# Kernel tuning notes

Measured on AMD Instinct MI355X. Metric: run time of the kernel, lower is better.

Reference implementation:

```python
import jax, jax.numpy as jnp
import numpy as np

MARGIN = 1.0
EPS = 1e-12


def setup_inputs() -> dict:
    key = jax.random.key(0)
    k1, k2, k3 = jax.random.split(key, 3)
    B, C, D = 16384, 500, 512
    features = jax.random.normal(k1, (B, D), dtype=jnp.float32)
    prototypes = jax.random.normal(k2, (C, D), dtype=jnp.float32)
    labels = jax.random.randint(k3, (B,), 0, C, dtype=jnp.int64)
    return {"features": features, "prototypes": prototypes, "labels": labels}


def reference(features, prototypes, labels):
    # Pairwise L2 distances [B, C] via the expanded form (no [B,C,D] intermediate)
    f2 = jnp.sum(features * features, axis=-1, keepdims=True)   # [B, 1]
    p2 = jnp.sum(prototypes * prototypes, axis=-1)               # [C]
    sq = f2 + p2 - 2.0 * (features @ prototypes.T)               # [B, C]
    dists = jnp.sqrt(jnp.maximum(sq, EPS))                       # [B, C]

    B, C = dists.shape
    d_pos = jnp.take_along_axis(dists, labels[:, None], axis=1)[:, 0]  # [B]
    pos_mask = jax.nn.one_hot(labels, C, dtype=bool)             # [B, C]
    d_neg_min = jnp.min(jnp.where(pos_mask, jnp.inf, dists), axis=-1)  # [B]

    loss = jnp.mean(jax.nn.relu(d_pos - d_neg_min + MARGIN))
    return loss
```

## Files before the change

### kernel.cpp

```cpp
#include <hip/hip_runtime.h>
#include <stdint.h>
#include <stddef.h>

#define BB 16384
#define CC 500
#define DD 512
#define PADC 512
#define LMARGIN 1.0f
#define EPSQ 1e-12f
#define NKC 16
#define ROWS 32

typedef __attribute__((ext_vector_type(8))) _Float16 f16x8;
typedef __attribute__((ext_vector_type(4))) _Float16 f16x4;
typedef __attribute__((ext_vector_type(4))) float f32x4;

#define GLOBAL_AS __attribute__((address_space(1)))
#define LDS_AS __attribute__((address_space(3)))

__device__ __forceinline__ void ld_lds16(const void* g, void* l) {
  __builtin_amdgcn_global_load_lds((const GLOBAL_AS void*)g, (LDS_AS void*)l, 16, 0, 0);
}

__global__ void prepP_kernel(const float* __restrict__ protos,
                             unsigned short* __restrict__ protoT,
                             float* __restrict__ p2,
                             float* __restrict__ out) {
  __shared__ float s_arr[16][17];
  const int cg = blockIdx.x;
  const int t = threadIdx.x;
  const int colin = t & 15;
  const int jb = t >> 4;
  const int col = cg * 16 + colin;
  if (cg == 0 && t == 0) out[0] = 0.f;
  float s = 0.f;
#pragma unroll
  for (int u = 0; u < 4; ++u) {
    const int j8 = jb + u * 16;
    const int kc = j8 >> 2, quad = j8 & 3;
    f32x4 a0 = {0.f, 0.f, 0.f, 0.f}, a1 = a0;
    if (col < CC) {
      const float* src = protos + (size_t)col * DD + j8 * 8;
      a0 = *(const f32x4*)src;
      a1 = *(const f32x4*)(src + 4);
    }
    f16x8 h;
#pragma unroll
    for (int uu = 0; uu < 4; ++uu) {
      h[uu] = (_Float16)a0[uu];
      h[uu + 4] = (_Float16)a1[uu];
      s = fmaf(a0[uu], a0[uu], s);
      s = fmaf(a1[uu], a1[uu], s);
    }
    *(f16x8*)(protoT + (size_t)(cg * 16 + kc) * 512 + (quad * 16 + colin) * 8) = h;
  }
  s_arr[colin][jb] = s;
  __syncthreads();
  if (t < 16) {
    float acc = 0.f;
#pragma unroll
    for (int i = 0; i < 16; ++i) acc += s_arr[t][i];
    p2[cg * 16 + t] = acc;
  }
}

__launch_bounds__(512, 4)
__global__ void main_kernel(const float* __restrict__ feat,
                            const unsigned short* __restrict__ protoT,
                            const float* __restrict__ p2,
                            const int* __restrict__ labels,
                            float* __restrict__ outp) {
  __shared__ __align__(16) unsigned char Afp[NKC * 4096];
  float* redM = (float*)&Afp[0];
  float* redP = (float*)&Afp[1024];
  float* f2l = (float*)&Afp[2048];

  const int tid = threadIdx.x;
  const int w = tid >> 6;
  const int lane = tid & 63;
  const int lane16 = lane & 15;
  const int quad = lane >> 4;
  const int r0 = blockIdx.x * ROWS;

  const char* bptr[4];
#pragma unroll
  for (int nt = 0; nt < 4; ++nt)
    bptr[nt] = (const char*)protoT + (size_t)(w * 64 + nt * 16) * 1024 + lane * 16;

  f16x8 bfr[3][4];
#pragma unroll
  for (int nt = 0; nt < 4; ++nt) {
    bfr[0][nt] = *(const f16x8*)(bptr[nt]);
    bfr[1][nt] = *(const f16x8*)(bptr[nt] + 1024);
  }

  const int l3 = lane >> 3, j8 = lane & 7;
  const float* aBase = feat + (size_t)(r0 + l3) * DD + ((j8 ^ l3) << 2);
  char* ldsBase = (char*)Afp + lane * 16;
  const int kcq0 = w >> 2, rb0 = w & 3;
  const int kcq1 = (8 + w) >> 2, rb1 = (8 + w) & 3;

#define DMA_Q(q)                                                            \
  do {                                                                      \
    int kcA = (q) * 4 + kcq0, kcB = (q) * 4 + kcq1;                         \
    ld_lds16(aBase + (size_t)(rb0 * 8) * DD + kcA * 32,                     \
             ldsBase + kcA * 4096 + rb0 * 1024);                            \
    ld_lds16(aBase + (size_t)(rb1 * 8) * DD + kcB * 32,                     \
             ldsBase + kcB * 4096 + rb1 * 1024);                            \
  } while (0)

  DMA_Q(0);

  f32x4 acc[2][4];
#pragma unroll
  for (int mt = 0; mt < 2; ++mt)
#pragma unroll
    for (int nt = 0; nt < 4; ++nt) acc[mt][nt] = (f32x4){0.f, 0.f, 0.f, 0.f};

  __syncthreads();

  const int r7 = lane16 & 7;
  const int c0 = ((quad * 2) ^ r7) * 16;
  const int c1 = ((quad * 2 + 1) ^ r7) * 16;
#pragma unroll
  for (int qi = 0; qi < 4; ++qi) {
    if (qi < 3) DMA_Q(qi + 1);
#pragma unroll
    for (int j = 0; j < 4; ++j) {
      const int kc = qi * 4 + j;
      if (kc + 2 < NKC) {
#pragma unroll
        for (int nt = 0; nt < 4; ++nt)
          bfr[(kc + 2) % 3][nt] =
              *(const f16x8*)(bptr[nt] + (size_t)(kc + 2) * 1024);
      }
      f16x8 af[2];
#pragma unroll
      for (int mt = 0; mt < 2; ++mt) {
        const unsigned char* ab = Afp + kc * 4096 + (mt * 16 + lane16) * 128;
        f32x4 x0 = *(const f32x4*)(ab + c0);
        f32x4 x1 = *(const f32x4*)(ab + c1);
        f16x8 a;
#pragma unroll
        for (int u = 0; u < 4; ++u) {
          a[u] = (_Float16)x0[u];
          a[u + 4] = (_Float16)x1[u];
        }
        af[mt] = a;
      }
#pragma unroll
      for (int mt = 0; mt < 2; ++mt)
#pragma unroll
        for (int nt = 0; nt < 4; ++nt)
          acc[mt][nt] = __builtin_amdgcn_mfma_f32_16x16x32_f16(
              af[mt], bfr[kc % 3][nt], acc[mt][nt], 0, 0, 0);
    }
    if (qi < 3) __syncthreads();
  }
#undef DMA_Q

  float s = 0.f;
  {
    const int frow = tid >> 4, fkc = tid & 15, t7 = tid & 7;
    const unsigned char* fb = Afp + fkc * 4096 + frow * 128;
#pragma unroll
    for (int si = 0; si < 8; ++si) {
      const int slot = ((si + t7) & 7) * 16;
      f32x4 v = *(const f32x4*)(fb + slot);
      s = fmaf(v[0], v[0], fmaf(v[1], v[1], fmaf(v[2], v[2], fmaf(v[3], v[3], s))));
    }
    s += __shfl_xor(s, 1, 64);
    s += __shfl_xor(s, 2, 64);
    s += __shfl_xor(s, 4, 64);
    s += __shfl_xor(s, 8, 64);
  }
  __syncthreads();
  if ((tid & 15) == 0) f2l[tid >> 4] = s;

  float p2v[4];
#pragma unroll
  for (int nt = 0; nt < 4; ++nt) p2v[nt] = p2[w * 64 + nt * 16 + lane16];

#pragma unroll
  for (int mt = 0; mt < 2; ++mt) {
#pragma unroll
    for (int i = 0; i < 4; ++i) {
      const int row = mt * 16 + quad * 4 + i;
      const int lb = labels[r0 + row];
      float qm = 1e30f, qp = -1e30f;
#pragma unroll
      for (int nt = 0; nt < 4; ++nt) {
        const int col = w * 64 + nt * 16 + lane16;
        float q = p2v[nt] - 2.f * acc[mt][nt][i];
        bool isPos = (col == lb);
        qp = fmaxf(qp, isPos ? q : -1e30f);
        qm = fminf(qm, (!isPos && col < CC) ? q : 1e30f);
      }
#pragma unroll
      for (int d = 1; d < 16; d <<= 1) {
        qm = fminf(qm, __shfl_xor(qm, d, 64));
        qp = fmaxf(qp, __shfl_xor(qp, d, 64));
      }
      if (lane16 == 0) {
        redM[row * 8 + w] = qm;
        redP[row * 8 + w] = qp;
      }
    }
  }
  __syncthreads();

  if (tid < ROWS) {
    float qm = 1e30f, qp = -1e30f;
#pragma unroll
    for (int j = 0; j < 8; ++j) {
      qm = fminf(qm, redM[tid * 8 + j]);
      qp = fmaxf(qp, redP[tid * 8 + j]);
    }
    float f2 = f2l[tid];
    float dn = sqrtf(fmaxf(f2 + qm, EPSQ));
    float dp = sqrtf(fmaxf(f2 + qp, EPSQ));
    float term = fmaxf(dp - dn + LMARGIN, 0.f);
#pragma unroll
    for (int d = 1; d < 32; d <<= 1) term += __shfl_xor(term, d, 64);
    if (tid == 0) atomicAdd(outp, term * (1.0f / BB));
  }
}

extern "C" void kernel_launch(void* const* d_in, const int* in_sizes, int n_in,
                              void* d_out, int out_size, void* d_ws, size_t ws_size,
                              hipStream_t stream) {
  const float* feat = (const float*)d_in[0];
  const float* protos = (const float*)d_in[1];
  const int* labels = (const int*)d_in[2];
  float* out = (float*)d_out;

  char* ws = (char*)d_ws;
  unsigned short* protoT = (unsigned short*)(ws);
  float* p2 = (float*)(ws + (512 << 10));

  prepP_kernel<<<32, 256, 0, stream>>>(protos, protoT, p2, out);
  main_kernel<<<BB / ROWS, 512, 0, stream>>>(feat, protoT, p2, labels, out);
}
```

Before: 94.82 us.

## Add dedicated producer wave feeding a 3-slot LDS ring with flag synchronization

Adds a ninth wave that acts as the sole producer. It streams feature tiles into a 3-slot LDS ring buffer with global_load_lds and signals each slot through shared-memory flags, while the eight compute waves spin-wait on those flags instead of block-wide barriers. The intent is to overlap feature loads with MFMA work and drop the per-quarter __syncthreads. The squared norm of each feature row is now accumulated inside the conversion loop, which removes the separate f2 reduction pass. LDS use falls from 64KB to about 48KB, but spin-wait sleeps and the extra wave add scheduling overhead and memory-ordering risk.

```diff
diff --git a/kernel.cpp b/kernel.cpp
--- a/kernel.cpp
+++ b/kernel.cpp
@@ -12,7 +12,6 @@
 #define ROWS 32
 
 typedef __attribute__((ext_vector_type(8))) _Float16 f16x8;
-typedef __attribute__((ext_vector_type(4))) _Float16 f16x4;
 typedef __attribute__((ext_vector_type(4))) float f32x4;
 
 #define GLOBAL_AS __attribute__((address_space(1)))
@@ -64,149 +63,157 @@
   }
 }
 
-__launch_bounds__(512, 4)
+__launch_bounds__(576, 4)
 __global__ void main_kernel(const float* __restrict__ feat,
                             const unsigned short* __restrict__ protoT,
                             const float* __restrict__ p2,
                             const int* __restrict__ labels,
                             float* __restrict__ outp) {
-  __shared__ __align__(16) unsigned char Afp[NKC * 4096];
-  float* redM = (float*)&Afp[0];
-  float* redP = (float*)&Afp[1024];
-  float* f2l = (float*)&Afp[2048];
+  __shared__ __align__(16) unsigned char Aring[3][16384];
+  __shared__ float redM[ROWS * 8], redP[ROWS * 8];
+  __shared__ float f2l[ROWS];
+  __shared__ int flagA[4];
+  __shared__ int done0;
 
   const int tid = threadIdx.x;
   const int w = tid >> 6;
   const int lane = tid & 63;
-  const int lane16 = lane & 15;
-  const int quad = lane >> 4;
   const int r0 = blockIdx.x * ROWS;
 
-  const char* bptr[4];
-#pragma unroll
-  for (int nt = 0; nt < 4; ++nt)
-    bptr[nt] = (const char*)protoT + (size_t)(w * 64 + nt * 16) * 1024 + lane * 16;
-
-  f16x8 bfr[3][4];
-#pragma unroll
-  for (int nt = 0; nt < 4; ++nt) {
-    bfr[0][nt] = *(const f16x8*)(bptr[nt]);
-    bfr[1][nt] = *(const f16x8*)(bptr[nt] + 1024);
-  }
-
-  const int l3 = lane >> 3, j8 = lane & 7;
-  const float* aBase = feat + (size_t)(r0 + l3) * DD + ((j8 ^ l3) << 2);
-  char* ldsBase = (char*)Afp + lane * 16;
-  const int kcq0 = w >> 2, rb0 = w & 3;
-  const int kcq1 = (8 + w) >> 2, rb1 = (8 + w) & 3;
-
-#define DMA_Q(q)                                                            \
-  do {                                                                      \
-    int kcA = (q) * 4 + kcq0, kcB = (q) * 4 + kcq1;                         \
-    ld_lds16(aBase + (size_t)(rb0 * 8) * DD + kcA * 32,                     \
-             ldsBase + kcA * 4096 + rb0 * 1024);                            \
-    ld_lds16(aBase + (size_t)(rb1 * 8) * DD + kcB * 32,                     \
-             ldsBase + kcB * 4096 + rb1 * 1024);                            \
-  } while (0)
-
-  DMA_Q(0);
-
-  f32x4 acc[2][4];
-#pragma unroll
-  for (int mt = 0; mt < 2; ++mt)
-#pragma unroll
-    for (int nt = 0; nt < 4; ++nt) acc[mt][nt] = (f32x4){0.f, 0.f, 0.f, 0.f};
-
+  if (tid == 0) {
+    flagA[0] = flagA[1] = flagA[2] = flagA[3] = 0;
+    done0 = 0;
+  }
   __syncthreads();
 
-  const int r7 = lane16 & 7;
-  const int c0 = ((quad * 2) ^ r7) * 16;
-  const int c1 = ((quad * 2 + 1) ^ r7) * 16;
-#pragma unroll
-  for (int qi = 0; qi < 4; ++qi) {
-    if (qi < 3) DMA_Q(qi + 1);
-#pragma unroll
-    for (int j = 0; j < 4; ++j) {
-      const int kc = qi * 4 + j;
-      if (kc + 2 < NKC) {
-#pragma unroll
-        for (int nt = 0; nt < 4; ++nt)
-          bfr[(kc + 2) % 3][nt] =
-              *(const f16x8*)(bptr[nt] + (size_t)(kc + 2) * 1024);
-      }
-      f16x8 af[2];
-#pragma unroll
-      for (int mt = 0; mt < 2; ++mt) {
-        const unsigned char* ab = Afp + kc * 4096 + (mt * 16 + lane16) * 128;
-        f32x4 x0 = *(const f32x4*)(ab + c0);
-        f32x4 x1 = *(const f32x4*)(ab + c1);
-        f16x8 a;
-#pragma unroll
-        for (int u = 0; u < 4; ++u) {
-          a[u] = (_Float16)x0[u];
-          a[u + 4] = (_Float16)x1[u];
-        }
-        af[mt] = a;
-      }
-#pragma unroll
-      for (int mt = 0; mt < 2; ++mt)
-#pragma unroll
-        for (int nt = 0; nt < 4; ++nt)
-          acc[mt][nt] = __builtin_amdgcn_mfma_f32_16x16x32_f16(
-              af[mt], bfr[kc % 3][nt], acc[mt][nt], 0, 0, 0);
-    }
-    if (qi < 3) __syncthreads();
-  }
-#undef DMA_Q
-
-  float s = 0.f;
-  {
-    const int frow = tid >> 4, fkc = tid & 15, t7 = tid & 7;
-    const unsigned char* fb = Afp + fkc * 4096 + frow * 128;
-#pragma unroll
-    for (int si = 0; si < 8; ++si) {
-      const int slot = ((si + t7) & 7) * 16;
-      f32x4 v = *(const f32x4*)(fb + slot);
-      s = fmaf(v[0], v[0], fmaf(v[1], v[1], fmaf(v[2], v[2], fmaf(v[3], v[3], s))));
-    }
-    s += __shfl_xor(s, 1, 64);
-    s += __shfl_xor(s, 2, 64);
-    s += __shfl_xor(s, 4, 64);
-    s += __shfl_xor(s, 8, 64);
-  }
-  __syncthreads();
-  if ((tid & 15) == 0) f2l[tid >> 4] = s;
-
-  float p2v[4];
-#pragma unroll
-  for (int nt = 0; nt < 4; ++nt) p2v[nt] = p2[w * 64 + nt * 16 + lane16];
-
-#pragma unroll
-  for (int mt = 0; mt < 2; ++mt) {
-#pragma unroll
-    for (int i = 0; i < 4; ++i) {
-      const int row = mt * 16 + quad * 4 + i;
-      const int lb = labels[r0 + row];
-      float qm = 1e30f, qp = -1e30f;
-#pragma unroll
-      for (int nt = 0; nt < 4; ++nt) {
-        const int col = w * 64 + nt * 16 + lane16;
-        float q = p2v[nt] - 2.f * acc[mt][nt][i];
-        bool isPos = (col == lb);
-        qp = fmaxf(qp, isPos ? q : -1e30f);
-        qm = fminf(qm, (!isPos && col < CC) ? q : 1e30f);
-      }
-#pragma unroll
-      for (int d = 1; d < 16; d <<= 1) {
-        qm = fminf(qm, __shfl_xor(qm, d, 64));
-        qp = fmaxf(qp, __shfl_xor(qp, d, 64));
-      }
-      if (lane16 == 0) {
-        redM[row * 8 + w] = qm;
-        redP[row * 8 + w] = qp;
-      }
-    }
-  }
+  if (w == 8) {
+    const int l3 = lane >> 3, j8 = lane & 7;
+    const float* aBase = feat + (size_t)(r0 + l3) * DD + ((j8 ^ l3) << 2);
+#pragma unroll 1
+    for (int q = 0; q < 4; ++q) {
+      if (q == 3) {
+        volatile int* vd = &done0;
+        while (*vd < 8) __builtin_amdgcn_s_sleep(8);
+      }
+      char* slot = (char*)&Aring[q % 3][0] + lane * 16;
+#pragma unroll
+      for (int kcl = 0; kcl < 4; ++kcl)
+#pragma unroll
+        for (int p = 0; p < 4; ++p)
+          ld_lds16(aBase + (size_t)(p * 8) * DD + (q * 4 + kcl) * 32,
+                   slot + kcl * 4096 + p * 1024);
+      __threadfence_block();
+      ((volatile int*)flagA)[q] = 1;
+    }
+  } else {
+    const int lane16 = lane & 15;
+    const int quad = lane >> 4;
+    const int r7 = lane16 & 7;
+    const int c0 = ((quad * 2) ^ r7) * 16;
+    const int c1 = ((quad * 2 + 1) ^ r7) * 16;
+
+    const char* bptr[4];
+#pragma unroll
+    for (int nt = 0; nt < 4; ++nt)
+      bptr[nt] = (const char*)protoT + (size_t)(w * 64 + nt * 16) * 1024 +
+                 lane * 16;
+    f16x8 bfr[3][4];
+#pragma unroll
+    for (int nt = 0; nt < 4; ++nt) {
+      bfr[0][nt] = *(const f16x8*)(bptr[nt]);
+      bfr[1][nt] = *(const f16x8*)(bptr[nt] + 1024);
+    }
+
+    f32x4 acc[2][4];
+#pragma unroll
+    for (int mt = 0; mt < 2; ++mt)
+#pragma unroll
+      for (int nt = 0; nt < 4; ++nt) acc[mt][nt] = (f32x4){0.f, 0.f, 0.f, 0.f};
+    float f2part[2] = {0.f, 0.f};
+
+#pragma unroll 1
+    for (int q = 0; q < 4; ++q) {
+      {
+        volatile int* vf = &flagA[q];
+        while (*vf == 0) __builtin_amdgcn_s_sleep(2);
+      }
+      const unsigned char* slot = &Aring[q % 3][0];
+#pragma unroll
+      for (int j = 0; j < 4; ++j) {
+        const int kc = q * 4 + j;
+        if (kc + 2 < NKC) {
+#pragma unroll
+          for (int nt = 0; nt < 4; ++nt)
+            bfr[(kc + 2) % 3][nt] =
+                *(const f16x8*)(bptr[nt] + (size_t)(kc + 2) * 1024);
+        }
+        f16x8 af[2];
+#pragma unroll
+        for (int mt = 0; mt < 2; ++mt) {
+          const unsigned char* ab = slot + j * 4096 + (mt * 16 + lane16) * 128;
+          f32x4 x0 = *(const f32x4*)(ab + c0);
+          f32x4 x1 = *(const f32x4*)(ab + c1);
+          f16x8 a;
+#pragma unroll
+          for (int u = 0; u < 4; ++u) {
+            a[u] = (_Float16)x0[u];
+            a[u + 4] = (_Float16)x1[u];
+            f2part[mt] = fmaf(x0[u], x0[u], f2part[mt]);
+            f2part[mt] = fmaf(x1[u], x1[u], f2part[mt]);
+          }
+          af[mt] = a;
+        }
+#pragma unroll
+        for (int mt = 0; mt < 2; ++mt)
+#pragma unroll
+          for (int nt = 0; nt < 4; ++nt)
+            acc[mt][nt] = __builtin_amdgcn_mfma_f32_16x16x32_f16(
+                af[mt], bfr[kc % 3][nt], acc[mt][nt], 0, 0, 0);
+      }
+      if (q == 0 && lane == 0) atomicAdd(&done0, 1);
+    }
+
+#pragma unroll
+    for (int mt = 0; mt < 2; ++mt) {
+      f2part[mt] += __shfl_xor(f2part[mt], 16, 64);
+      f2part[mt] += __shfl_xor(f2part[mt], 32, 64);
+    }
+    if (w == 0 && quad == 0) {
+      f2l[lane16] = f2part[0];
+      f2l[16 + lane16] = f2part[1];
+    }
+
+    float p2v[4];
+#pragma unroll
+    for (int nt = 0; nt < 4; ++nt) p2v[nt] = p2[w * 64 + nt * 16 + lane16];
+#pragma unroll
+    for (int mt = 0; mt < 2; ++mt) {
+#pragma unroll
+      for (int i = 0; i < 4; ++i) {
+        const int row = mt * 16 + quad * 4 + i;
+        const int lb = labels[r0 + row];
+        float qm = 1e30f, qp = -1e30f;
+#pragma unroll
+        for (int nt = 0; nt < 4; ++nt) {
+          const int col = w * 64 + nt * 16 + lane16;
+          float qv = p2v[nt] - 2.f * acc[mt][nt][i];
+          bool isPos = (col == lb);
+          qp = fmaxf(qp, isPos ? qv : -1e30f);
+          qm = fminf(qm, (!isPos && col < CC) ? qv : 1e30f);
+        }
+#pragma unroll
+        for (int d = 1; d < 16; d <<= 1) {
+          qm = fminf(qm, __shfl_xor(qm, d, 64));
+          qp = fmaxf(qp, __shfl_xor(qp, d, 64));
+        }
+        if (lane16 == 0) {
+          redM[row * 8 + w] = qm;
+          redP[row * 8 + w] = qp;
+        }
+      }
+    }
+  }
+
   __syncthreads();
 
   if (tid < ROWS) {
@@ -239,5 +246,5 @@
   float* p2 = (float*)(ws + (512 << 10));
 
   prepP_kernel<<<32, 256, 0, stream>>>(protos, protoT, p2, out);
-  main_kernel<<<BB / ROWS, 512, 0, stream>>>(feat, protoT, p2, labels, out);
-}
+  main_kernel<<<BB / ROWS, 576, 0, stream>>>(feat, protoT, p2, labels, out);
+}
```

Result: slower. 191.5 us (+102.0%).
